# Kernel optimization log

Hardware: AMD Instinct MI355X
Metric: run time of the kernel (lower is better)

The kernel has to match this reference:

```python
import jax, jax.numpy as jnp
import numpy as np

B_, L_, D_ = 2, 1024, 512   # batch, seq_len, dim
H_ = 8                      # num_heads, head_dim = 64
Q_ = 64                     # chunk size for the chunked semi-separable scan


def setup_inputs() -> dict:
    key = jax.random.key(0)
    ks = jax.random.split(key, 7)
    s = 1.0 / np.sqrt(D_)   # torch nn.Linear default init bound
    x = jax.random.normal(ks[0], (B_, L_, D_), dtype=jnp.float32)
    W_A = jax.random.uniform(ks[1], (D_, D_), jnp.float32, -s, s)
    b_A = jax.random.uniform(ks[2], (D_,), jnp.float32, -s, s)
    W_B = jax.random.uniform(ks[3], (D_, D_), jnp.float32, -s, s)
    b_B = jax.random.uniform(ks[4], (D_,), jnp.float32, -s, s)
    W_C = jax.random.uniform(ks[5], (D_, D_), jnp.float32, -s, s)
    b_C = jax.random.uniform(ks[6], (D_,), jnp.float32, -s, s)
    return {"x": x, "W_A": W_A, "b_A": b_A, "W_B": W_B, "b_B": b_B,
            "W_C": W_C, "b_C": b_C}


def _semi_separable_T(x, W_A, b_A, W_B, b_B, W_C, b_C):
    """T_ij = sum_d C_{i,d} * (prod_{k=j+1}^{i-1} A_{k,d}) * B_{j,d}, j <= i.

    Computed in log space with Mamba2-style chunking: all exponent
    differences are <= 0, so exp() underflows to 0 (the true limit)
    instead of producing inf/nan as a naive cumprod-quotient would.
    """
    B, L, D = x.shape
    H = H_
    Dh = D // H
    Q = Q_
    nc = L // Q
    NEG = -jnp.inf

    A = jax.nn.sigmoid(x @ W_A.T + b_A)    # [B,L,D], values in (0,1)
    Bf = x @ W_B.T + b_B
    C = x @ W_C.T + b_C

    def heads(t):
        return t.reshape(B, L, H, Dh).transpose(0, 2, 1, 3)  # [B,H,L,Dh]

    A, Bf, C = heads(A), heads(Bf), heads(C)

    S = jnp.cumsum(jnp.log(A), axis=2)                       # S[k] = sum_{0..k} log A
    Sm1 = jnp.concatenate([jnp.zeros_like(S[:, :, :1]), S[:, :, :-1]], axis=2)
    # prod_{k=j+1}^{i-1} A_k = exp(Sm1[i] - S[j])  for i >= j+1 (==1 at i=j+1)

    def chunk(t):
        return t.reshape(B, H, nc, Q, Dh)

    Sc, Sm1c, Bc, Cc = chunk(S), chunk(Sm1), chunk(Bf), chunk(C)

    qi = jnp.arange(Q)[:, None]
    ki = jnp.arange(Q)[None, :]
    lower = (qi > ki)[None, None, None, :, :, None]
    diag = (qi == ki)[None, None, None, :, :, None]

    # ---- diagonal blocks (within-chunk, strictly lower + diagonal) ----
    diff = Sm1c[:, :, :, :, None, :] - Sc[:, :, :, None, :, :]  # [B,H,nc,Q,Q,Dh], <=0 where q>k
    dec = jnp.where(lower, diff, jnp.where(diag, 0.0, NEG))     # q==k -> prod=1
    Tdiag = jnp.einsum('bhmqd,bhmqkd,bhmkd->bhmqk', Cc, jnp.exp(dec), Bc)

    # ---- cross blocks (chunk m queries vs chunk n<m keys) ----
    E = Sc[:, :, :, -1, :]                                      # S at last index of each chunk
    Eprev = jnp.concatenate([jnp.zeros_like(E[:, :, :1]), E[:, :, :-1]], axis=2)
    qf = Cc * jnp.exp(Sm1c - Eprev[:, :, :, None, :])           # exponent <= 0
    kf = Bc * jnp.exp(E[:, :, :, None, :] - Sc)                 # exponent <= 0
    mi = jnp.arange(nc)[:, None]
    ni = jnp.arange(nc)[None, :]
    cross_mask = (ni < mi)[None, None, :, :, None]
    Dcross = jnp.exp(jnp.where(cross_mask,
                               Eprev[:, :, :, None, :] - E[:, :, None, :, :],
                               NEG))                            # [B,H,nc,nc,Dh]
    T = jnp.einsum('bhmqd,bhmnd,bhnkd->bhmqnk', qf, Dcross, kf)

    idx = jnp.arange(nc)
    T = T.at[:, :, idx, :, idx, :].set(jnp.moveaxis(Tdiag, 2, 0))
    return T.reshape(B, H, L, L)


def reference(x, W_A, b_A, W_B, b_B, W_C, b_C):
    return _semi_separable_T(x, W_A, b_A, W_B, b_B, W_C, b_C)
```

## Files before the change

kernel.cpp:

```cpp
#include <hip/hip_runtime.h>
#include <math.h>

#define BB 2
#define LL 1024
#define DD 512
#define HH 8
#define DHD 64
#define QQ 64
#define NCC 16

typedef __attribute__((ext_vector_type(8))) short s8b;
typedef __attribute__((ext_vector_type(4))) float f4;

__device__ __forceinline__ void gld16(const void* g, void* l) {
    __builtin_amdgcn_global_load_lds(
        (const __attribute__((address_space(1))) unsigned int*)g,
        (__attribute__((address_space(3))) unsigned int*)l, 16, 0, 0);
}

__device__ __forceinline__ void bf16split(float f, unsigned short& h, unsigned short& l) {
    unsigned u  = __float_as_uint(f);
    unsigned hb = (u + 0x7FFFu + ((u >> 16) & 1u)) & 0xFFFF0000u;
    float fh = __uint_as_float(hb);
    float fl = f - fh;
    unsigned ul = __float_as_uint(fl);
    unsigned lb = (ul + 0x7FFFu + ((ul >> 16) & 1u)) >> 16;
    h = (unsigned short)(hb >> 16);
    l = (unsigned short)lb;
}

__device__ __forceinline__ unsigned pk2(unsigned short a, unsigned short b) {
    return (unsigned)a | ((unsigned)b << 16);
}

__global__ __launch_bounds__(256) void convert_split(
    const float* __restrict__ x, const float* __restrict__ Wa,
    const float* __restrict__ Wb, const float* __restrict__ Wc,
    unsigned short* __restrict__ xh, unsigned short* __restrict__ xl,
    unsigned short* __restrict__ wh, unsigned short* __restrict__ wl)
{
    const int g = blockIdx.x * 256 + threadIdx.x;
    const float* src;
    unsigned short *dh, *dl;
    if (g < 262144) {
        const size_t off = (size_t)g * 4;
        src = x + off; dh = xh + off; dl = xl + off;
    } else {
        const size_t j = (size_t)(g - 262144) * 4;
        const int wsel = (int)(j >> 18);
        const size_t r = j & 262143;
        src = (wsel == 0 ? Wa : (wsel == 1 ? Wb : Wc)) + r;
        dh = wh + j; dl = wl + j;
    }
    const float4 v = *(const float4*)src;
    const float f[4] = {v.x, v.y, v.z, v.w};
    unsigned short h[4], l[4];
    #pragma unroll
    for (int i = 0; i < 4; ++i) bf16split(f[i], h[i], l[i]);
    *(uint2*)dh = make_uint2(pk2(h[0], h[1]), pk2(h[2], h[3]));
    *(uint2*)dl = make_uint2(pk2(l[0], l[1]), pk2(l[2], l[3]));
}

__global__ __launch_bounds__(512) void gemm3_fused(
    const unsigned short* __restrict__ xh, const unsigned short* __restrict__ xl,
    const unsigned short* __restrict__ wh, const unsigned short* __restrict__ wl,
    const float* __restrict__ ba, const float* __restrict__ bb, const float* __restrict__ bc,
    float* __restrict__ logA, float* __restrict__ Bf, float* __restrict__ Cf,
    float* __restrict__ csum)
{
    __shared__ unsigned char lds[65536];
    __shared__ float csv[64];

    const int bm = blockIdx.x >> 3;
    const int bn = blockIdx.x & 7;
    const int m0 = bm << 6, o0 = bn << 6;
    const int t = threadIdx.x, wv = t >> 6, ln = t & 63;
    const int l15 = ln & 15, l4 = ln >> 4;
    const int wr = (wv >> 2) << 5;
    const int wc = (wv & 3) << 4;

    const unsigned short* hp = (wv < 2) ? xh : wh + (size_t)((wv - 2) >> 1) * 262144;
    const unsigned short* lp = (wv < 2) ? xl : wl + (size_t)((wv - 2) >> 1) * 262144;
    const unsigned short* sp2 = ((wv & 1) ? lp : hp) + (size_t)((wv < 2) ? m0 : o0) * DD;
    const int abase = wv * 4096;

    const int rl = ln >> 2;
    const int sl = ln & 3;
    size_t gofs[4];
    #pragma unroll
    for (int s = 0; s < 4; ++s) {
        const int rowg = s * 16 + rl;
        const int kfc  = sl ^ ((rowg >> 1) & 3);
        gofs[s] = (size_t)rowg * DD + kfc * 8;
    }

    f4 acc[3][2] = {};

    auto STAGE = [&](int buf, int kt) {
        unsigned char* base = lds + buf * 32768 + abase;
        #pragma unroll
        for (int s = 0; s < 4; ++s)
            gld16(sp2 + kt + gofs[s], base + s * 1024);
    };

    auto ldso = [&](int row, int kg) {
        return row * 64 + ((kg ^ ((row >> 1) & 3)) << 4);
    };

    auto COMPUTE = [&](int buf) {
        const unsigned char* base = lds + buf * 32768;
        const s8b ah0 = *(const s8b*)(base + 0*4096 + ldso(wr      + l15, l4));
        const s8b ah1 = *(const s8b*)(base + 0*4096 + ldso(wr + 16 + l15, l4));
        const s8b al0 = *(const s8b*)(base + 1*4096 + ldso(wr      + l15, l4));
        const s8b al1 = *(const s8b*)(base + 1*4096 + ldso(wr + 16 + l15, l4));
        #pragma unroll
        for (int s = 0; s < 3; ++s) {
            const s8b bh = *(const s8b*)(base + (2 + 2*s)*4096 + ldso(wc + l15, l4));
            const s8b bl = *(const s8b*)(base + (3 + 2*s)*4096 + ldso(wc + l15, l4));
            acc[s][0] = __builtin_amdgcn_mfma_f32_16x16x32_bf16(ah0, bh, acc[s][0], 0, 0, 0);
            acc[s][1] = __builtin_amdgcn_mfma_f32_16x16x32_bf16(ah1, bh, acc[s][1], 0, 0, 0);
            acc[s][0] = __builtin_amdgcn_mfma_f32_16x16x32_bf16(ah0, bl, acc[s][0], 0, 0, 0);
            acc[s][1] = __builtin_amdgcn_mfma_f32_16x16x32_bf16(ah1, bl, acc[s][1], 0, 0, 0);
            acc[s][0] = __builtin_amdgcn_mfma_f32_16x16x32_bf16(al0, bh, acc[s][0], 0, 0, 0);
            acc[s][1] = __builtin_amdgcn_mfma_f32_16x16x32_bf16(al1, bh, acc[s][1], 0, 0, 0);
        }
    };

    STAGE(0, 0);
    __syncthreads();
    int cur = 0;
    for (int it = 0; it < 16; ++it) {
        if (it < 15) STAGE(cur ^ 1, (it + 1) * 32);
        COMPUTE(cur);
        __syncthreads();
        cur ^= 1;
    }

    const int col = o0 + wc + l15;
    const float bva = ba[col], bvb = bb[col], bvc = bc[col];
    float asum = 0.f;
    #pragma unroll
    for (int ms = 0; ms < 2; ++ms) {
        const int row0 = m0 + wr + ms * 16 + l4 * 4;
        #pragma unroll
        for (int r = 0; r < 4; ++r) {
            const size_t o = (size_t)(row0 + r) * DD + col;
            float va = acc[0][ms][r] + bva;
            va = fminf(va, 0.f) - log1pf(__expf(-fabsf(va)));
            logA[o] = va;
            asum += va;
            Bf[o] = acc[1][ms][r] + bvb;
            Cf[o] = acc[2][ms][r] + bvc;
        }
    }

    asum += __shfl_xor(asum, 16);
    asum += __shfl_xor(asum, 32);
    if (wv < 4 && l4 == 0) csv[wc + l15] = asum;
    __syncthreads();
    if (wv >= 4 && l4 == 0) {
        const int blkc = (((bm >> 4) * 8 + bn) << 4) + (bm & 15);
        csum[(size_t)blkc * DHD + wc + l15] = csv[wc + l15] + asum;
    }
}

__global__ __launch_bounds__(256) void scan_diag(
    const float* __restrict__ logA, const float* __restrict__ Bf,
    const float* __restrict__ Cf, const float* __restrict__ csum,
    float* __restrict__ qf, float* __restrict__ kf,
    float* __restrict__ coff, float* __restrict__ out)
{
    __shared__ float part[4][DHD];
    __shared__ float smA[DHD][65];
    __shared__ float smB[DHD][65];
    __shared__ float smC[DHD][65];

    const int blk = blockIdx.x;
    const int bh = blk >> 4, c = blk & 15;
    const int b = bh >> 3, h = bh & 7;
    const int t = threadIdx.x;
    const int d = t & 63, w = t >> 6;

    const size_t gbase = (size_t)(b * LL + c * QQ + w * 16) * DD + h * DHD + d;
    float lar[16];
    float ps = 0.f;
    #pragma unroll
    for (int i = 0; i < 16; ++i) {
        lar[i] = logA[gbase + (size_t)i * DD];
        ps += lar[i];
    }
    part[w][d] = ps;
    __syncthreads();

    const size_t cs0 = ((size_t)bh << 4) * DHD + d;
    float off = 0.f;
    for (int cc = 0; cc < c; ++cc) off += csum[cs0 + (size_t)cc * DHD];
    const float tot = part[0][d] + part[1][d] + part[2][d] + part[3][d];
    if (t < DHD) {
        coff[((size_t)bh * 17 + c) * DHD + t] = off;
        if (c == NCC - 1) coff[((size_t)bh * 17 + 16) * DHD + t] = off + tot;
    }

    float run = 0.f;
    for (int ww = 0; ww < 4; ++ww) if (ww < w) run += part[ww][d];

    const size_t hbase = ((size_t)bh * LL + c * QQ + w * 16) * DHD + d;
    #pragma unroll
    for (int i = 0; i < 16; ++i) {
        const size_t gi = gbase + (size_t)i * DD;
        const float cv = Cf[gi];
        const float bv = Bf[gi];
        qf[hbase + (size_t)i * DHD] = cv * __expf(run);
        run += lar[i];
        const int rloc = w * 16 + i;
        smC[d][rloc] = run;
        smA[d][rloc] = cv;
        smB[d][rloc] = bv;
        kf[hbase + (size_t)i * DHD] = bv * __expf(tot - run);
    }
    __syncthreads();

    const int q0 = ((t >> 4) & 15) << 2;
    const int k0 = (t & 15) << 2;

    float acc[4][4] = {};
    if (q0 + 3 >= k0) {
        #pragma unroll 2
        for (int dd = 0; dd < DHD; ++dd) {
            const float4 cq = *(const float4*)&smA[dd][q0];
            const float4 bk = *(const float4*)&smB[dd][k0];
            const float4 sk = *(const float4*)&smC[dd][k0];
            const float cqa[4] = {cq.x, cq.y, cq.z, cq.w};
            const float bka[4] = {bk.x, bk.y, bk.z, bk.w};
            const float ska[4] = {sk.x, sk.y, sk.z, sk.w};
            float s1a[4];
            #pragma unroll
            for (int i = 0; i < 4; ++i) {
                const int qi = q0 + i;
                s1a[i] = (qi == 0) ? 0.f : smC[dd][qi - 1];
            }
            #pragma unroll
            for (int i = 0; i < 4; ++i) {
                #pragma unroll
                for (int j = 0; j < 4; ++j) {
                    const int qi = q0 + i, kj = k0 + j;
                    const float wgt = (qi > kj) ? __expf(s1a[i] - ska[j])
                                                : ((qi == kj) ? 1.f : 0.f);
                    acc[i][j] += cqa[i] * wgt * bka[j];
                }
            }
        }
    }
    const size_t outrow0 = ((size_t)bh * LL + (size_t)c * QQ) * LL + (size_t)c * QQ;
    #pragma unroll
    for (int i = 0; i < 4; ++i)
        *(float4*)&out[outrow0 + (size_t)(q0 + i) * LL + k0] =
            make_float4(acc[i][0], acc[i][1], acc[i][2], acc[i][3]);
}

__global__ __launch_bounds__(256) void band_row(
    const float* __restrict__ qf, const float* __restrict__ kf,
    const float* __restrict__ coff, float* __restrict__ out)
{
    __shared__ unsigned char lds[49152];
    unsigned char* const l_qh = lds;
    unsigned char* const l_ql = lds + 8192;

    const int half = blockIdx.x & 1;
    const int m    = (blockIdx.x >> 1) & 15;
    const int bh   = blockIdx.x >> 5;
    const int n0   = half << 3;

    const int t  = threadIdx.x;
    const int wv = t >> 6;
    const int ln = t & 63;
    const int l15 = ln & 15;
    const int l4  = ln >> 4;
    const int wr = (wv >> 1) << 5;
    const int wc = (wv & 1) << 5;

    const int srow = t >> 2;
    const int skc  = (t & 3) << 4;
    const int slot0 = skc >> 3;

    const size_t cb = (size_t)bh * 17 * DHD;
    const size_t outbase = ((size_t)bh * LL + (size_t)m * QQ) * LL;

    for (int n = (m >= n0 ? m + 1 : n0); n < n0 + 8; ++n) {
        const size_t ob = outbase + (size_t)srow * LL + (size_t)n * QQ + skc;
        const float4 z = make_float4(0.f, 0.f, 0.f, 0.f);
        *(float4*)&out[ob + 0]  = z;
        *(float4*)&out[ob + 4]  = z;
        *(float4*)&out[ob + 8]  = z;
        *(float4*)&out[ob + 12] = z;
    }

    const int ne = (m < n0 + 8) ? m : (n0 + 8);
    if (n0 >= ne) return;

    float cm[16];
    #pragma unroll
    for (int g = 0; g < 4; ++g) {
        const float4 a = *(const float4*)&coff[cb + (size_t)m * DHD + skc + g * 4];
        cm[g*4+0]=a.x; cm[g*4+1]=a.y; cm[g*4+2]=a.z; cm[g*4+3]=a.w;
    }

    {
        const size_t qb = ((size_t)bh * LL + (size_t)m * QQ + srow) * DHD + skc;
        float v[16];
        #pragma unroll
        for (int g = 0; g < 4; ++g) {
            const float4 x4 = *(const float4*)&qf[qb + g * 4];
            v[g*4+0]=x4.x; v[g*4+1]=x4.y; v[g*4+2]=x4.z; v[g*4+3]=x4.w;
        }
        unsigned short h[16], l[16];
        #pragma unroll
        for (int i = 0; i < 16; ++i) bf16split(v[i], h[i], l[i]);
        *(uint4*)(l_qh + slot0*1024 + srow*16) =
            make_uint4(pk2(h[0],h[1]), pk2(h[2],h[3]), pk2(h[4],h[5]), pk2(h[6],h[7]));
        *(uint4*)(l_qh + (slot0+1)*1024 + srow*16) =
            make_uint4(pk2(h[8],h[9]), pk2(h[10],h[11]), pk2(h[12],h[13]), pk2(h[14],h[15]));
        *(uint4*)(l_ql + slot0*1024 + srow*16) =
            make_uint4(pk2(l[0],l[1]), pk2(l[2],l[3]), pk2(l[4],l[5]), pk2(l[6],l[7]));
        *(uint4*)(l_ql + (slot0+1)*1024 + srow*16) =
            make_uint4(pk2(l[8],l[9]), pk2(l[10],l[11]), pk2(l[12],l[13]), pk2(l[14],l[15]));
    }

    auto LOAD_K = [&](int n, float* vk, float* vc) {
        const size_t kb = ((size_t)bh * LL + (size_t)n * QQ + srow) * DHD + skc;
        #pragma unroll
        for (int g = 0; g < 4; ++g) {
            const float4 x4 = *(const float4*)&kf[kb + g * 4];
            vk[g*4+0]=x4.x; vk[g*4+1]=x4.y; vk[g*4+2]=x4.z; vk[g*4+3]=x4.w;
            const float4 c4 = *(const float4*)&coff[cb + (size_t)(n + 1) * DHD + skc + g * 4];
            vc[g*4+0]=c4.x; vc[g*4+1]=c4.y; vc[g*4+2]=c4.z; vc[g*4+3]=c4.w;
        }
    };

    auto WRITE_K = [&](int buf, const float* vk, const float* vc) {
        unsigned char* const kh_b = lds + 16384 + buf * 16384;
        unsigned char* const kl_b = kh_b + 8192;
        float v[16];
        #pragma unroll
        for (int i = 0; i < 16; ++i)
            v[i] = vk[i] * __expf(cm[i] - vc[i]);
        unsigned short h[16], l[16];
        #pragma unroll
        for (int i = 0; i < 16; ++i) bf16split(v[i], h[i], l[i]);
        *(uint4*)(kh_b + slot0*1024 + srow*16) =
            make_uint4(pk2(h[0],h[1]), pk2(h[2],h[3]), pk2(h[4],h[5]), pk2(h[6],h[7]));
        *(uint4*)(kh_b + (slot0+1)*1024 + srow*16) =
            make_uint4(pk2(h[8],h[9]), pk2(h[10],h[11]), pk2(h[12],h[13]), pk2(h[14],h[15]));
        *(uint4*)(kl_b + slot0*1024 + srow*16) =
            make_uint4(pk2(l[0],l[1]), pk2(l[2],l[3]), pk2(l[4],l[5]), pk2(l[6],l[7]));
        *(uint4*)(kl_b + (slot0+1)*1024 + srow*16) =
            make_uint4(pk2(l[8],l[9]), pk2(l[10],l[11]), pk2(l[12],l[13]), pk2(l[14],l[15]));
    };

    {
        float pk0[16], pc0[16];
        LOAD_K(n0, pk0, pc0);
        WRITE_K(0, pk0, pc0);
    }
    __syncthreads();

    int cur = 0;
    for (int n = n0; n < ne; ++n) {
        float nk[16], nc[16];
        const bool pre = (n + 1 < ne);
        if (pre) LOAD_K(n + 1, nk, nc);

        const unsigned char* const kh_b = lds + 16384 + cur * 16384;
        const unsigned char* const kl_b = kh_b + 8192;

        f4 acc[2][2] = {};
        #pragma unroll
        for (int ks = 0; ks < 2; ++ks) {
            const int ka = (ks * 4 + l4) * 1024;
            const s8b kh0 = *(const s8b*)(kh_b + ka + (wr      + l15) * 16);
            const s8b kh1 = *(const s8b*)(kh_b + ka + (wr + 16 + l15) * 16);
            const s8b kl0 = *(const s8b*)(kl_b + ka + (wr      + l15) * 16);
            const s8b kl1 = *(const s8b*)(kl_b + ka + (wr + 16 + l15) * 16);
            const s8b qh0 = *(const s8b*)(l_qh + ka + (wc      + l15) * 16);
            const s8b qh1 = *(const s8b*)(l_qh + ka + (wc + 16 + l15) * 16);
            const s8b ql0 = *(const s8b*)(l_ql + ka + (wc      + l15) * 16);
            const s8b ql1 = *(const s8b*)(l_ql + ka + (wc + 16 + l15) * 16);

            acc[0][0] = __builtin_amdgcn_mfma_f32_16x16x32_bf16(kh0, qh0, acc[0][0], 0, 0, 0);
            acc[0][1] = __builtin_amdgcn_mfma_f32_16x16x32_bf16(kh0, qh1, acc[0][1], 0, 0, 0);
            acc[1][0] = __builtin_amdgcn_mfma_f32_16x16x32_bf16(kh1, qh0, acc[1][0], 0, 0, 0);
            acc[1][1] = __builtin_amdgcn_mfma_f32_16x16x32_bf16(kh1, qh1, acc[1][1], 0, 0, 0);
            acc[0][0] = __builtin_amdgcn_mfma_f32_16x16x32_bf16(kh0, ql0, acc[0][0], 0, 0, 0);
            acc[0][1] = __builtin_amdgcn_mfma_f32_16x16x32_bf16(kh0, ql1, acc[0][1], 0, 0, 0);
            acc[1][0] = __builtin_amdgcn_mfma_f32_16x16x32_bf16(kh1, ql0, acc[1][0], 0, 0, 0);
            acc[1][1] = __builtin_amdgcn_mfma_f32_16x16x32_bf16(kh1, ql1, acc[1][1], 0, 0, 0);
            acc[0][0] = __builtin_amdgcn_mfma_f32_16x16x32_bf16(kl0, qh0, acc[0][0], 0, 0, 0);
            acc[0][1] = __builtin_amdgcn_mfma_f32_16x16x32_bf16(kl0, qh1, acc[0][1], 0, 0, 0);
            acc[1][0] = __builtin_amdgcn_mfma_f32_16x16x32_bf16(kl1, qh0, acc[1][0], 0, 0, 0);
            acc[1][1] = __builtin_amdgcn_mfma_f32_16x16x32_bf16(kl1, qh1, acc[1][1], 0, 0, 0);
        }

        #pragma unroll
        for (int ms = 0; ms < 2; ++ms) {
            #pragma unroll
            for (int ns = 0; ns < 2; ++ns) {
                const int q  = wc + ns * 16 + l15;
                const int k0 = wr + ms * 16 + l4 * 4;
                *(float4*)&out[outbase + (size_t)q * LL + (size_t)n * QQ + k0] =
                    make_float4(acc[ms][ns][0], acc[ms][ns][1], acc[ms][ns][2], acc[ms][ns][3]);
            }
        }

        if (pre) WRITE_K(cur ^ 1, nk, nc);

        __syncthreads();
        cur ^= 1;
    }
}

extern "C" void kernel_launch(void* const* d_in, const int* in_sizes, int n_in,
                              void* d_out, int out_size, void* d_ws, size_t ws_size,
                              hipStream_t stream) {
    const float* x  = (const float*)d_in[0];
    const float* Wa = (const float*)d_in[1];
    const float* ba = (const float*)d_in[2];
    const float* Wb = (const float*)d_in[3];
    const float* bb = (const float*)d_in[4];
    const float* Wc = (const float*)d_in[5];
    const float* bc = (const float*)d_in[6];
    float* out = (float*)d_out;
    float* ws  = (float*)d_ws;

    const size_t NBLD = (size_t)BB * LL * DD;
    float* logA = ws;
    float* Bf   = ws + 1 * NBLD;
    float* Cf   = ws + 2 * NBLD;
    float* qf   = ws + 4 * NBLD;
    float* kf   = ws + 5 * NBLD;
    float* coff = ws + 6 * NBLD;
    float* csum = coff + (size_t)BB * HH * 17 * DHD;

    unsigned short* xh  = (unsigned short*)(ws + 3 * NBLD);
    unsigned short* xl  = xh + 1048576;
    unsigned short* whp = xl + 1048576;
    unsigned short* wlp = whp + 786432;

    convert_split<<<1792, 256, 0, stream>>>(x, Wa, Wb, Wc, xh, xl, whp, wlp);
    gemm3_fused<<<256, 512, 0, stream>>>(xh, xl, whp, wlp, ba, bb, bc, logA, Bf, Cf, csum);
    scan_diag<<<BB * HH * NCC, 256, 0, stream>>>(logA, Bf, Cf, csum, qf, kf, coff, out);
    band_row<<<BB * HH * NCC * 2, 256, 0, stream>>>(qf, kf, coff, out);
}
```

Measured before the change: 81.49 us.

## Fuse bf16 hi/lo split into GEMM staging, drop separate convert kernel

```diff
diff --git a/kernel.cpp b/kernel.cpp
--- a/kernel.cpp
+++ b/kernel.cpp
@@ -11,12 +11,6 @@
 
 typedef __attribute__((ext_vector_type(8))) short s8b;
 typedef __attribute__((ext_vector_type(4))) float f4;
-
-__device__ __forceinline__ void gld16(const void* g, void* l) {
-    __builtin_amdgcn_global_load_lds(
-        (const __attribute__((address_space(1))) unsigned int*)g,
-        (__attribute__((address_space(3))) unsigned int*)l, 16, 0, 0);
-}
 
 __device__ __forceinline__ void bf16split(float f, unsigned short& h, unsigned short& l) {
     unsigned u  = __float_as_uint(f);
@@ -33,38 +27,11 @@
     return (unsigned)a | ((unsigned)b << 16);
 }
 
-__global__ __launch_bounds__(256) void convert_split(
-    const float* __restrict__ x, const float* __restrict__ Wa,
-    const float* __restrict__ Wb, const float* __restrict__ Wc,
-    unsigned short* __restrict__ xh, unsigned short* __restrict__ xl,
-    unsigned short* __restrict__ wh, unsigned short* __restrict__ wl)
-{
-    const int g = blockIdx.x * 256 + threadIdx.x;
-    const float* src;
-    unsigned short *dh, *dl;
-    if (g < 262144) {
-        const size_t off = (size_t)g * 4;
-        src = x + off; dh = xh + off; dl = xl + off;
-    } else {
-        const size_t j = (size_t)(g - 262144) * 4;
-        const int wsel = (int)(j >> 18);
-        const size_t r = j & 262143;
-        src = (wsel == 0 ? Wa : (wsel == 1 ? Wb : Wc)) + r;
-        dh = wh + j; dl = wl + j;
-    }
-    const float4 v = *(const float4*)src;
-    const float f[4] = {v.x, v.y, v.z, v.w};
-    unsigned short h[4], l[4];
-    #pragma unroll
-    for (int i = 0; i < 4; ++i) bf16split(f[i], h[i], l[i]);
-    *(uint2*)dh = make_uint2(pk2(h[0], h[1]), pk2(h[2], h[3]));
-    *(uint2*)dl = make_uint2(pk2(l[0], l[1]), pk2(l[2], l[3]));
-}
-
 __global__ __launch_bounds__(512) void gemm3_fused(
-    const unsigned short* __restrict__ xh, const unsigned short* __restrict__ xl,
-    const unsigned short* __restrict__ wh, const unsigned short* __restrict__ wl,
-    const float* __restrict__ ba, const float* __restrict__ bb, const float* __restrict__ bc,
+    const float* __restrict__ x,
+    const float* __restrict__ Wa, const float* __restrict__ ba,
+    const float* __restrict__ Wb, const float* __restrict__ bb,
+    const float* __restrict__ Wc, const float* __restrict__ bc,
     float* __restrict__ logA, float* __restrict__ Bf, float* __restrict__ Cf,
     float* __restrict__ csum)
 {
@@ -79,28 +46,41 @@
     const int wr = (wv >> 2) << 5;
     const int wc = (wv & 3) << 4;
 
-    const unsigned short* hp = (wv < 2) ? xh : wh + (size_t)((wv - 2) >> 1) * 262144;
-    const unsigned short* lp = (wv < 2) ? xl : wl + (size_t)((wv - 2) >> 1) * 262144;
-    const unsigned short* sp2 = ((wv & 1) ? lp : hp) + (size_t)((wv < 2) ? m0 : o0) * DD;
-    const int abase = wv * 4096;
-
-    const int rl = ln >> 2;
-    const int sl = ln & 3;
-    size_t gofs[4];
-    #pragma unroll
-    for (int s = 0; s < 4; ++s) {
-        const int rowg = s * 16 + rl;
-        const int kfc  = sl ^ ((rowg >> 1) & 3);
-        gofs[s] = (size_t)rowg * DD + kfc * 8;
-    }
+    const int src_id = wv >> 1;
+    const float* srcp =
+        (src_id == 0) ? x + (size_t)m0 * DD :
+        ((src_id == 1) ? Wa : (src_id == 2) ? Wb : Wc) + (size_t)o0 * DD;
+    const int roff = ((wv & 1) << 5) + (ln >> 1);
+    const int ksh  = (ln & 1) << 4;
+    const int swz  = (roff >> 1) & 3;
+    const int sA   = ((ksh >> 3) + 0) ^ swz;
+    const int sB   = ((ksh >> 3) + 1) ^ swz;
+    const size_t srow = (size_t)roff * DD + ksh;
+    const int hiBase = (src_id * 2) * 4096 + roff * 64;
 
     f4 acc[3][2] = {};
 
     auto STAGE = [&](int buf, int kt) {
-        unsigned char* base = lds + buf * 32768 + abase;
-        #pragma unroll
-        for (int s = 0; s < 4; ++s)
-            gld16(sp2 + kt + gofs[s], base + s * 1024);
+        const float* p = srcp + srow + kt;
+        const float4 f0 = *(const float4*)(p + 0);
+        const float4 f1 = *(const float4*)(p + 4);
+        const float4 f2 = *(const float4*)(p + 8);
+        const float4 f3 = *(const float4*)(p + 12);
+        const float v[16] = {f0.x,f0.y,f0.z,f0.w, f1.x,f1.y,f1.z,f1.w,
+                             f2.x,f2.y,f2.z,f2.w, f3.x,f3.y,f3.z,f3.w};
+        unsigned short h[16], l[16];
+        #pragma unroll
+        for (int i = 0; i < 16; ++i) bf16split(v[i], h[i], l[i]);
+        unsigned char* bh = lds + buf * 32768 + hiBase;
+        unsigned char* bl = bh + 4096;
+        *(uint4*)(bh + sA * 16) = make_uint4(pk2(h[0],h[1]),  pk2(h[2],h[3]),
+                                             pk2(h[4],h[5]),  pk2(h[6],h[7]));
+        *(uint4*)(bh + sB * 16) = make_uint4(pk2(h[8],h[9]),  pk2(h[10],h[11]),
+                                             pk2(h[12],h[13]),pk2(h[14],h[15]));
+        *(uint4*)(bl + sA * 16) = make_uint4(pk2(l[0],l[1]),  pk2(l[2],l[3]),
+                                             pk2(l[4],l[5]),  pk2(l[6],l[7]));
+        *(uint4*)(bl + sB * 16) = make_uint4(pk2(l[8],l[9]),  pk2(l[10],l[11]),
+                                             pk2(l[12],l[13]),pk2(l[14],l[15]));
     };
 
     auto ldso = [&](int row, int kg) {
@@ -440,13 +420,7 @@
     float* coff = ws + 6 * NBLD;
     float* csum = coff + (size_t)BB * HH * 17 * DHD;
 
-    unsigned short* xh  = (unsigned short*)(ws + 3 * NBLD);
-    unsigned short* xl  = xh + 1048576;
-    unsigned short* whp = xl + 1048576;
-    unsigned short* wlp = whp + 786432;
-
-    convert_split<<<1792, 256, 0, stream>>>(x, Wa, Wb, Wc, xh, xl, whp, wlp);
-    gemm3_fused<<<256, 512, 0, stream>>>(xh, xl, whp, wlp, ba, bb, bc, logA, Bf, Cf, csum);
+    gemm3_fused<<<256, 512, 0, stream>>>(x, Wa, ba, Wb, bb, Wc, bc, logA, Bf, Cf, csum);
     scan_diag<<<BB * HH * NCC, 256, 0, stream>>>(logA, Bf, Cf, csum, qf, kf, coff, out);
     band_row<<<BB * HH * NCC * 2, 256, 0, stream>>>(qf, kf, coff, out);
 }
```

Result: no change. 81.98 us (+0.6%).
